# Kernel tuning notes

Measured on AMD Instinct MI355X. Metric: run time of the kernel, lower is better.

The kernel has to match this reference:

```python
import jax, jax.numpy as jnp
import numpy as np

IN_DIM = 256
OUT_DIM = 256


def setup_inputs() -> dict:
    key = jax.random.key(0)
    k1, k2, k3, k4 = jax.random.split(key, 4)
    B, N = 8, 2048
    X = jax.random.normal(k1, (B, N, IN_DIM), dtype=jnp.float32)
    adj = jax.random.uniform(k2, (B, N, N), dtype=jnp.float32)
    # nn.Linear(input_dim, output_dim): W is [out, in], bias [out]
    bound = 1.0 / np.sqrt(IN_DIM)
    W = jax.random.uniform(k3, (OUT_DIM, IN_DIM), minval=-bound, maxval=bound, dtype=jnp.float32)
    b = jax.random.uniform(k4, (OUT_DIM,), minval=-bound, maxval=bound, dtype=jnp.float32)
    return {"X": X, "adj": adj, "W": W, "b": b}


def reference(X, adj, W, b):
    N = adj.shape[-1]
    # adj_hat = adj + I
    adj_hat = adj + jnp.eye(N, dtype=adj.dtype)
    # D^{-1/2} A_hat D^{-1/2}: diag matmuls are just row/col scaling
    d = jnp.sum(adj_hat, axis=-1) ** -0.5  # [B, N]
    adj_norm = d[..., :, None] * adj_hat * d[..., None, :]
    # aggregate then linear + relu
    H = jnp.matmul(adj_norm, X)  # [B, N, F_in]
    out = jnp.einsum('bnf,of->bno', H, W) + b
    return jax.nn.relu(out)
```

## Files before the change

### kernel.cpp

```cpp
#include <hip/hip_runtime.h>
#include <stdint.h>

typedef __attribute__((ext_vector_type(8))) short bf16x8;
typedef __attribute__((ext_vector_type(8))) unsigned short u16x8;
typedef __attribute__((ext_vector_type(4))) float f32x4;
typedef unsigned short u16;

constexpr int NN = 2048, NF = 256;

__device__ inline u16 f2bf(float f) {
  uint32_t u = __builtin_bit_cast(uint32_t, f);
  uint32_t r = (u + 0x7FFFu + ((u >> 16) & 1u)) >> 16;
  return (u16)r;
}
__device__ inline float bf2f(u16 h) {
  uint32_t u = ((uint32_t)h) << 16;
  return __builtin_bit_cast(float, u);
}

__device__ inline void gload_lds16(const void* g, void* l) {
  __builtin_amdgcn_global_load_lds(
      (const __attribute__((address_space(1))) uint32_t*)g,
      (__attribute__((address_space(3))) uint32_t*)l,
      16, 0, 0);
}

__global__ __launch_bounds__(256) void k_rowsum(const float* __restrict__ adj,
                                                float* __restrict__ d,
                                                const float* __restrict__ W,
                                                u16* __restrict__ Wb) {
  if (blockIdx.x >= 16384) {
    int i = (blockIdx.x - 16384) * 256 + threadIdx.x;
    float4 v = ((const float4*)W)[i];
    ushort4 o;
    o.x = f2bf(v.x); o.y = f2bf(v.y); o.z = f2bf(v.z); o.w = f2bf(v.w);
    *(ushort4*)(Wb + (size_t)i * 4) = o;
    return;
  }
  int row = blockIdx.x;
  const float4* p = (const float4*)(adj + (size_t)row * NN);
  float s = 0.f;
#pragma unroll
  for (int c = 0; c < 2; ++c) {
    float4 v = p[threadIdx.x + 256 * c];
    s += v.x + v.y + v.z + v.w;
  }
#pragma unroll
  for (int off = 32; off > 0; off >>= 1) s += __shfl_down(s, off, 64);
  __shared__ float red[4];
  int lane = threadIdx.x & 63, w = threadIdx.x >> 6;
  if (lane == 0) red[w] = s;
  __syncthreads();
  if (threadIdx.x == 0) {
    float t = red[0] + red[1] + red[2] + red[3] + 1.0f;
    d[row] = 1.0f / sqrtf(t);
  }
}

__global__ __launch_bounds__(256) void k_xprep(const float* __restrict__ X,
                                               const float* __restrict__ d,
                                               u16* __restrict__ XpT) {
  int jt = blockIdx.x, ft = blockIdx.y, b = blockIdx.z;
  int j0 = jt * 64, f0 = ft * 64;
  __shared__ u16 T[64][66];
  int t = threadIdx.x;
#pragma unroll
  for (int s = 0; s < 4; ++s) {
    int q = s * 256 + t;
    int r = q >> 4, c4 = q & 15;
    int j = j0 + r;
    float dv = d[b * NN + j];
    float4 v = *(const float4*)(X + ((size_t)(b * NN + j)) * NF + f0 + c4 * 4);
    T[r][c4 * 4 + 0] = f2bf(v.x * dv);
    T[r][c4 * 4 + 1] = f2bf(v.y * dv);
    T[r][c4 * 4 + 2] = f2bf(v.z * dv);
    T[r][c4 * 4 + 3] = f2bf(v.w * dv);
  }
  __syncthreads();
#pragma unroll
  for (int s = 0; s < 4; ++s) {
    int q = s * 256 + t;
    int fr = q >> 4, c4 = q & 15;
    ushort4 o;
    o.x = T[c4 * 4 + 0][fr]; o.y = T[c4 * 4 + 1][fr];
    o.z = T[c4 * 4 + 2][fr]; o.w = T[c4 * 4 + 3][fr];
    *(ushort4*)(XpT + ((size_t)(b * NF + f0 + fr)) * NN + j0 + c4 * 4) = o;
  }
}

#define BBASE 24576

#define MFMA8(AB, BB)                                                          \
  {                                                                            \
    bf16x8 af0 = *(const bf16x8*)((AB) + aoff0);                               \
    bf16x8 af1 = *(const bf16x8*)((AB) + aoff0 + 1024);                        \
    bf16x8 b0 = *(const bf16x8*)((BB) + boff0);                                \
    bf16x8 b1 = *(const bf16x8*)((BB) + boff0 + 1024);                         \
    bf16x8 b2 = *(const bf16x8*)((BB) + boff0 + 2048);                         \
    bf16x8 b3 = *(const bf16x8*)((BB) + boff0 + 3072);                         \
    asm volatile("s_waitcnt lgkmcnt(0)" ::: "memory");                         \
    __builtin_amdgcn_sched_barrier(0);                                         \
    __builtin_amdgcn_s_setprio(1);                                             \
    acc[0][0] = __builtin_amdgcn_mfma_f32_16x16x32_bf16(af0, b0, acc[0][0], 0, 0, 0); \
    acc[0][1] = __builtin_amdgcn_mfma_f32_16x16x32_bf16(af0, b1, acc[0][1], 0, 0, 0); \
    acc[0][2] = __builtin_amdgcn_mfma_f32_16x16x32_bf16(af0, b2, acc[0][2], 0, 0, 0); \
    acc[0][3] = __builtin_amdgcn_mfma_f32_16x16x32_bf16(af0, b3, acc[0][3], 0, 0, 0); \
    acc[1][0] = __builtin_amdgcn_mfma_f32_16x16x32_bf16(af1, b0, acc[1][0], 0, 0, 0); \
    acc[1][1] = __builtin_amdgcn_mfma_f32_16x16x32_bf16(af1, b1, acc[1][1], 0, 0, 0); \
    acc[1][2] = __builtin_amdgcn_mfma_f32_16x16x32_bf16(af1, b2, acc[1][2], 0, 0, 0); \
    acc[1][3] = __builtin_amdgcn_mfma_f32_16x16x32_bf16(af1, b3, acc[1][3], 0, 0, 0); \
    __builtin_amdgcn_s_setprio(0);                                             \
  }

#define PAIR(G, RG, WG, SN, SW, BR0, BR1, BW0, BW1, VMC0, VMC1, IA, WA, IB0, IB1) \
  {                                                                            \
                                                 \
    if (IB0) {                                                                 \
      gload_lds16(b_src0 + (size_t)(2 * (G) + 2) * 32,                         \
                  smem + BBASE + (BW0) * 16384 + bw0);                         \
      gload_lds16(b_src1 + (size_t)(2 * (G) + 2) * 32,                         \
                  smem + BBASE + (BW0) * 16384 + bw1);                         \
    }                                                                          \
    if (IA) {                                                                  \
      aN0[SN] = *(const float4*)(a_gsrc + (size_t)((G) + 4) * 64);             \
      aN1[SN] = *(const float4*)(a_gsrc + (size_t)((G) + 4) * 64 + 4);         \
    }                                                                          \
    __builtin_amdgcn_sched_barrier(0);                                         \
    asm volatile("s_waitcnt vmcnt(" VMC0 ") lgkmcnt(0)" ::: "memory");         \
    __builtin_amdgcn_sched_barrier(0);                                         \
    __builtin_amdgcn_s_barrier();                                              \
    __builtin_amdgcn_sched_barrier(0);                                         \
    MFMA8(smem + (RG) * 8192, smem + BBASE + (BR0) * 16384)                    \
    __builtin_amdgcn_sched_barrier(0);                                         \
    if (WA) {                                                                  \
      float4 c0 = aN0[SW], c1 = aN1[SW];                                       \
      u16x8 pk;                                                                \
      pk[0] = f2bf(c0.x); pk[1] = f2bf(c0.y); pk[2] = f2bf(c0.z);              \
      pk[3] = f2bf(c0.w); pk[4] = f2bf(c1.x); pk[5] = f2bf(c1.y);              \
      pk[6] = f2bf(c1.z); pk[7] = f2bf(c1.w);                                  \
      *(u16x8*)(smem + (WG) * 8192 + a_ldst) = pk;                             \
    }                                                                          \
    __builtin_amdgcn_sched_barrier(0);                                         \
                                                \
    if (IB1) {                                                                 \
      gload_lds16(b_src0 + (size_t)(2 * (G) + 3) * 32,                         \
                  smem + BBASE + (BW1) * 16384 + bw0);                         \
      gload_lds16(b_src1 + (size_t)(2 * (G) + 3) * 32,                         \
                  smem + BBASE + (BW1) * 16384 + bw1);                         \
    }                                                                          \
    __builtin_amdgcn_sched_barrier(0);                                         \
    asm volatile("s_waitcnt vmcnt(" VMC1 ") lgkmcnt(0)" ::: "memory");         \
    __builtin_amdgcn_sched_barrier(0);                                         \
    __builtin_amdgcn_s_barrier();                                              \
    __builtin_amdgcn_sched_barrier(0);                                         \
    MFMA8(smem + (RG) * 8192 + 4096, smem + BBASE + (BR1) * 16384)             \
    __builtin_amdgcn_sched_barrier(0);                                         \
  }

__global__ __launch_bounds__(512, 2) void k_fused(
    const float* __restrict__ adj, const u16* __restrict__ XpT,
    const float* __restrict__ dsc, const u16* __restrict__ Wb,
    const float* __restrict__ bias, float* __restrict__ out) {
  int flat = blockIdx.x;
  int b = flat & 7, mt = flat >> 3;
  int i0 = mt * 64;

  __shared__ __align__(16) char smem[90112];
  u16* Hs = (u16*)smem;

  int t = threadIdx.x;
  int lane = t & 63, w = t >> 6;
  int l15 = lane & 15, l4 = lane >> 4;
  int wr = w >> 2, wc = w & 3;

  const float* adjf = adj + ((size_t)b * NN + i0) * NN;
  const u16* XpTb = XpT + (size_t)b * NF * NN;

  int rA = t >> 3, kc = t & 7;
  const float* a_gsrc = adjf + (size_t)rA * NN + kc * 8;
  int a_ldst = (kc >> 2) * 4096 + rA * 64 + (((kc & 3) ^ ((rA >> 1) & 3)) << 4);

  int n0s = t >> 2, c0s = t & 3;
  const u16* b_src0 = XpTb + (size_t)n0s * NN + ((c0s ^ ((n0s >> 1) & 3)) << 3);
  int s1 = 512 + t;
  int n1s = s1 >> 2, c1s = s1 & 3;
  const u16* b_src1 = XpTb + (size_t)n1s * NN + ((c1s ^ ((n1s >> 1) & 3)) << 3);
  int bw0 = w << 10;
  int bw1 = 8192 + (w << 10);

  int swz = (l4 ^ ((l15 >> 1) & 3)) << 4;
  int aoff0 = wr * 2048 + l15 * 64 + swz;
  int boff0 = (wc * 64 + l15) * 64 + swz;

  f32x4 acc[2][4] = {};
  float4 aN0[3], aN1[3];

  {
    float4 p0a = *(const float4*)(a_gsrc);
    float4 p0b = *(const float4*)(a_gsrc + 4);
    float4 p1a = *(const float4*)(a_gsrc + 64);
    float4 p1b = *(const float4*)(a_gsrc + 68);
    __builtin_amdgcn_sched_barrier(0);
    gload_lds16(b_src0, smem + BBASE + bw0);
    gload_lds16(b_src1, smem + BBASE + bw1);
    gload_lds16(b_src0 + 32, smem + BBASE + 16384 + bw0);
    gload_lds16(b_src1 + 32, smem + BBASE + 16384 + bw1);
    __builtin_amdgcn_sched_barrier(0);
    aN0[1] = *(const float4*)(a_gsrc + 128);
    aN1[1] = *(const float4*)(a_gsrc + 132);
    aN0[2] = *(const float4*)(a_gsrc + 192);
    aN1[2] = *(const float4*)(a_gsrc + 196);
    __builtin_amdgcn_sched_barrier(0);
    u16x8 pk;
    pk[0] = f2bf(p0a.x); pk[1] = f2bf(p0a.y); pk[2] = f2bf(p0a.z);
    pk[3] = f2bf(p0a.w); pk[4] = f2bf(p0b.x); pk[5] = f2bf(p0b.y);
    pk[6] = f2bf(p0b.z); pk[7] = f2bf(p0b.w);
    *(u16x8*)(smem + a_ldst) = pk;
    pk[0] = f2bf(p1a.x); pk[1] = f2bf(p1a.y); pk[2] = f2bf(p1a.z);
    pk[3] = f2bf(p1a.w); pk[4] = f2bf(p1b.x); pk[5] = f2bf(p1b.y);
    pk[6] = f2bf(p1b.z); pk[7] = f2bf(p1b.w);
    *(u16x8*)(smem + 8192 + a_ldst) = pk;
    __builtin_amdgcn_sched_barrier(0);
  }

  for (int gb = 0; gb < 24; gb += 6) {
    PAIR(gb + 0, 0, 2, 0, 1, 0, 1, 2, 3, "8", "6", 1, 1, 1, 1)
    PAIR(gb + 1, 1, 0, 1, 2, 2, 3, 0, 1, "8", "6", 1, 1, 1, 1)
    PAIR(gb + 2, 2, 1, 2, 0, 0, 1, 2, 3, "8", "6", 1, 1, 1, 1)
    PAIR(gb + 3, 0, 2, 0, 1, 2, 3, 0, 1, "8", "6", 1, 1, 1, 1)
    PAIR(gb + 4, 1, 0, 1, 2, 0, 1, 2, 3, "8", "6", 1, 1, 1, 1)
    PAIR(gb + 5, 2, 1, 2, 0, 2, 3, 0, 1, "8", "6", 1, 1, 1, 1)
  }
  PAIR(24, 0, 2, 0, 1, 0, 1, 2, 3, "8", "6", 1, 1, 1, 1)
  PAIR(25, 1, 0, 1, 2, 2, 3, 0, 1, "8", "6", 1, 1, 1, 1)
  PAIR(26, 2, 1, 2, 0, 0, 1, 2, 3, "8", "6", 1, 1, 1, 1)
  PAIR(27, 0, 2, 0, 1, 2, 3, 0, 1, "8", "6", 1, 1, 1, 1)
  PAIR(28, 1, 0, 1, 2, 0, 1, 2, 3, "6", "4", 0, 1, 1, 1)
  PAIR(29, 2, 1, 2, 0, 2, 3, 0, 1, "4", "4", 0, 1, 1, 1)
  PAIR(30, 0, 2, 0, 1, 0, 1, 2, 3, "4", "4", 0, 0, 1, 1)
  PAIR(31, 1, 0, 1, 2, 2, 3, 0, 1, "2", "0", 0, 0, 0, 0)

  __syncthreads();

  const float* db = dsc + b * NN;
#pragma unroll
  for (int mi = 0; mi < 2; ++mi) {
#pragma unroll
    for (int ni = 0; ni < 4; ++ni) {
      int f = wc * 64 + ni * 16 + l15;
      ushort4 xv = *(const ushort4*)(XpTb + (size_t)f * NN + i0 +
                                     wr * 32 + mi * 16 + l4 * 4);
#pragma unroll
      for (int qq = 0; qq < 4; ++qq) {
        int il = wr * 32 + mi * 16 + l4 * 4 + qq;
        float dv = db[i0 + il];
        float xpv = bf2f(((const u16*)&xv)[qq]);
        float hv = dv * (acc[mi][ni][qq] + xpv);
        Hs[il * 264 + f] = f2bf(hv);
      }
    }
  }
  __syncthreads();

  f32x4 acc2[2][4] = {};
#pragma unroll
  for (int kk = 0; kk < 256; kk += 32) {
    bf16x8 a2[2], b2[4];
#pragma unroll
    for (int mi = 0; mi < 2; ++mi) {
      int r = wr * 32 + mi * 16 + l15;
      a2[mi] = *(const bf16x8*)&Hs[r * 264 + kk + l4 * 8];
    }
#pragma unroll
    for (int ni = 0; ni < 4; ++ni) {
      int o = wc * 64 + ni * 16 + l15;
      b2[ni] = *(const bf16x8*)&Wb[(size_t)o * 256 + kk + l4 * 8];
    }
#pragma unroll
    for (int mi = 0; mi < 2; ++mi)
#pragma unroll
      for (int ni = 0; ni < 4; ++ni)
        acc2[mi][ni] = __builtin_amdgcn_mfma_f32_16x16x32_bf16(a2[mi], b2[ni],
                                                               acc2[mi][ni], 0, 0, 0);
  }

  float* outb = out + ((size_t)b * NN + i0) * NF;
#pragma unroll
  for (int mi = 0; mi < 2; ++mi) {
#pragma unroll
    for (int qq = 0; qq < 4; ++qq) {
      int il = wr * 32 + mi * 16 + l4 * 4 + qq;
#pragma unroll
      for (int ni = 0; ni < 4; ++ni) {
        int o = wc * 64 + ni * 16 + l15;
        float v = acc2[mi][ni][qq] + bias[o];
        outb[(size_t)il * NF + o] = fmaxf(v, 0.f);
      }
    }
  }
}

extern "C" void kernel_launch(void* const* d_in, const int* in_sizes, int n_in,
                              void* d_out, int out_size, void* d_ws, size_t ws_size,
                              hipStream_t stream) {
  const float* X    = (const float*)d_in[0];
  const float* adj  = (const float*)d_in[1];
  const float* W    = (const float*)d_in[2];
  const float* bias = (const float*)d_in[3];
  float* out = (float*)d_out;

  char* ws = (char*)d_ws;
  float* dsc = (float*)(ws);
  u16*   Wb  = (u16*)(ws + 65536);
  u16*   XpT = (u16*)(ws + 262144);

  k_rowsum<<<dim3(16448), dim3(256), 0, stream>>>(adj, dsc, W, Wb);
  k_xprep<<<dim3(32, 4, 8), dim3(256), 0, stream>>>(X, dsc, XpT);
  k_fused<<<dim3(256), dim3(512), 0, stream>>>(adj, XpT, dsc, Wb, bias, out);
}
```

Baseline: 73.14 us.

## Deepen B-operand LDS pipeline from four to six stages

Grows the shared-memory ring for the bf16 X tiles from four to six 16KB slots. The prologue now preloads four B sub-tiles, and each PAIR prefetches two sub-tiles further ahead, with the vmcnt waits and the unrolled schedule retuned to match. The aim is to hide more global-load latency behind the MFMA work. The cost is 120KB of LDS per block, which likely no longer allows two 512-thread blocks per CU as the launch bounds request, so occupancy may drop.

New measurement: 74.20 us. Within noise of the previous version (+1.4%).

```diff
diff --git a/kernel.cpp b/kernel.cpp
--- a/kernel.cpp
+++ b/kernel.cpp
@@ -112,18 +112,18 @@
     __builtin_amdgcn_s_setprio(0);                                             \
   }
 
-#define PAIR(G, RG, WG, SN, SW, BR0, BR1, BW0, BW1, VMC0, VMC1, IA, WA, IB0, IB1) \
+#define PAIR(G, RG, WG, SN, SW, BR0, BR1, BW0, BW1, VMC0, VMC1, IA, WA, IB)    \
   {                                                                            \
-                                                 \
-    if (IB0) {                                                                 \
-      gload_lds16(b_src0 + (size_t)(2 * (G) + 2) * 32,                         \
-                  smem + BBASE + (BW0) * 16384 + bw0);                         \
-      gload_lds16(b_src1 + (size_t)(2 * (G) + 2) * 32,                         \
-                  smem + BBASE + (BW0) * 16384 + bw1);                         \
-    }                                                                          \
+                   \
     if (IA) {                                                                  \
       aN0[SN] = *(const float4*)(a_gsrc + (size_t)((G) + 4) * 64);             \
       aN1[SN] = *(const float4*)(a_gsrc + (size_t)((G) + 4) * 64 + 4);         \
+    }                                                                          \
+    if (IB) {                                                                  \
+      gload_lds16(b_src0 + (size_t)(2 * (G) + 4) * 32,                         \
+                  smem + BBASE + (BW0) * 16384 + bw0);                         \
+      gload_lds16(b_src1 + (size_t)(2 * (G) + 4) * 32,                         \
+                  smem + BBASE + (BW0) * 16384 + bw1);                         \
     }                                                                          \
     __builtin_amdgcn_sched_barrier(0);                                         \
     asm volatile("s_waitcnt vmcnt(" VMC0 ") lgkmcnt(0)" ::: "memory");         \
@@ -142,10 +142,10 @@
     }                                                                          \
     __builtin_amdgcn_sched_barrier(0);                                         \
                                                 \
-    if (IB1) {                                                                 \
-      gload_lds16(b_src0 + (size_t)(2 * (G) + 3) * 32,                         \
+    if (IB) {                                                                  \
+      gload_lds16(b_src0 + (size_t)(2 * (G) + 5) * 32,                         \
                   smem + BBASE + (BW1) * 16384 + bw0);                         \
-      gload_lds16(b_src1 + (size_t)(2 * (G) + 3) * 32,                         \
+      gload_lds16(b_src1 + (size_t)(2 * (G) + 5) * 32,                         \
                   smem + BBASE + (BW1) * 16384 + bw1);                         \
     }                                                                          \
     __builtin_amdgcn_sched_barrier(0);                                         \
@@ -165,7 +165,7 @@
   int b = flat & 7, mt = flat >> 3;
   int i0 = mt * 64;
 
-  __shared__ __align__(16) char smem[90112];
+  __shared__ __align__(16) char smem[122880];
   u16* Hs = (u16*)smem;
 
   int t = threadIdx.x;
@@ -205,6 +205,10 @@
     gload_lds16(b_src1, smem + BBASE + bw1);
     gload_lds16(b_src0 + 32, smem + BBASE + 16384 + bw0);
     gload_lds16(b_src1 + 32, smem + BBASE + 16384 + bw1);
+    gload_lds16(b_src0 + 64, smem + BBASE + 32768 + bw0);
+    gload_lds16(b_src1 + 64, smem + BBASE + 32768 + bw1);
+    gload_lds16(b_src0 + 96, smem + BBASE + 49152 + bw0);
+    gload_lds16(b_src1 + 96, smem + BBASE + 49152 + bw1);
     __builtin_amdgcn_sched_barrier(0);
     aN0[1] = *(const float4*)(a_gsrc + 128);
     aN1[1] = *(const float4*)(a_gsrc + 132);
@@ -223,22 +227,16 @@
     __builtin_amdgcn_sched_barrier(0);
   }
 
-  for (int gb = 0; gb < 24; gb += 6) {
-    PAIR(gb + 0, 0, 2, 0, 1, 0, 1, 2, 3, "8", "6", 1, 1, 1, 1)
-    PAIR(gb + 1, 1, 0, 1, 2, 2, 3, 0, 1, "8", "6", 1, 1, 1, 1)
-    PAIR(gb + 2, 2, 1, 2, 0, 0, 1, 2, 3, "8", "6", 1, 1, 1, 1)
-    PAIR(gb + 3, 0, 2, 0, 1, 2, 3, 0, 1, "8", "6", 1, 1, 1, 1)
-    PAIR(gb + 4, 1, 0, 1, 2, 0, 1, 2, 3, "8", "6", 1, 1, 1, 1)
-    PAIR(gb + 5, 2, 1, 2, 0, 2, 3, 0, 1, "8", "6", 1, 1, 1, 1)
-  }
-  PAIR(24, 0, 2, 0, 1, 0, 1, 2, 3, "8", "6", 1, 1, 1, 1)
-  PAIR(25, 1, 0, 1, 2, 2, 3, 0, 1, "8", "6", 1, 1, 1, 1)
-  PAIR(26, 2, 1, 2, 0, 0, 1, 2, 3, "8", "6", 1, 1, 1, 1)
-  PAIR(27, 0, 2, 0, 1, 2, 3, 0, 1, "8", "6", 1, 1, 1, 1)
-  PAIR(28, 1, 0, 1, 2, 0, 1, 2, 3, "6", "4", 0, 1, 1, 1)
-  PAIR(29, 2, 1, 2, 0, 2, 3, 0, 1, "4", "4", 0, 1, 1, 1)
-  PAIR(30, 0, 2, 0, 1, 0, 1, 2, 3, "4", "4", 0, 0, 1, 1)
-  PAIR(31, 1, 0, 1, 2, 2, 3, 0, 1, "2", "0", 0, 0, 0, 0)
+  for (int gb = 0; gb < 27; gb += 3) {
+    PAIR(gb + 0, 0, 2, 0, 1, 0, 1, 4, 5, "12", "12", 1, 1, 1)
+    PAIR(gb + 1, 1, 0, 1, 2, 2, 3, 0, 1, "12", "12", 1, 1, 1)
+    PAIR(gb + 2, 2, 1, 2, 0, 4, 5, 2, 3, "12", "12", 1, 1, 1)
+  }
+  PAIR(27, 0, 2, 0, 1, 0, 1, 4, 5, "12", "12", 1, 1, 1)
+  PAIR(28, 1, 0, 1, 2, 2, 3, 0, 1, "10", "10", 0, 1, 1)
+  PAIR(29, 2, 1, 2, 0, 4, 5, 2, 3, "8", "8", 0, 1, 1)
+  PAIR(30, 0, 2, 0, 1, 0, 1, 4, 5, "6", "4", 0, 0, 0)
+  PAIR(31, 1, 0, 1, 2, 2, 3, 0, 1, "2", "0", 0, 0, 0)
 
   __syncthreads();
 
```

## Merge prep kernels by moving column scaling into fused GEMM A-load

Applied to the files above, without the earlier changes.

The X transpose/convert no longer depends on the degree vector, so it is merged with the rowsum and W conversion into a single pre-kernel, which removes one launch and its serialization. The column scaling d_j is applied instead to adj elements as they are converted to bf16 inside the fused kernel, which adds extra loads of d and multiplies to the main loop. The main loop is restructured to process two B k-slices per step with one barrier instead of two, using a larger B ring and more LDS. The self-loop term is adjusted to dv*dv*x.

Measured after the change: 78.08 us. +6.8%, slower.

```diff
diff --git a/kernel.cpp b/kernel.cpp
--- a/kernel.cpp
+++ b/kernel.cpp
@@ -25,147 +25,154 @@
       16, 0, 0);
 }
 
-__global__ __launch_bounds__(256) void k_rowsum(const float* __restrict__ adj,
-                                                float* __restrict__ d,
-                                                const float* __restrict__ W,
-                                                u16* __restrict__ Wb) {
-  if (blockIdx.x >= 16384) {
-    int i = (blockIdx.x - 16384) * 256 + threadIdx.x;
+__global__ __launch_bounds__(256) void k_pre(const float* __restrict__ adj,
+                                             float* __restrict__ d,
+                                             const float* __restrict__ X,
+                                             u16* __restrict__ YpT,
+                                             const float* __restrict__ W,
+                                             u16* __restrict__ Wb) {
+  __shared__ u16 T[64][66];
+  __shared__ float red[4];
+  int bx = blockIdx.x, t = threadIdx.x;
+
+  if (bx < 1024) {
+    int jt = bx & 31, ft = (bx >> 5) & 3, b = bx >> 7;
+    int j0 = jt * 64, f0 = ft * 64;
+#pragma unroll
+    for (int s = 0; s < 4; ++s) {
+      int q = s * 256 + t;
+      int r = q >> 4, c4 = q & 15;
+      int j = j0 + r;
+      float4 v = *(const float4*)(X + ((size_t)(b * NN + j)) * NF + f0 + c4 * 4);
+      T[r][c4 * 4 + 0] = f2bf(v.x);
+      T[r][c4 * 4 + 1] = f2bf(v.y);
+      T[r][c4 * 4 + 2] = f2bf(v.z);
+      T[r][c4 * 4 + 3] = f2bf(v.w);
+    }
+    __syncthreads();
+#pragma unroll
+    for (int s = 0; s < 4; ++s) {
+      int q = s * 256 + t;
+      int fr = q >> 4, c4 = q & 15;
+      ushort4 o;
+      o.x = T[c4 * 4 + 0][fr]; o.y = T[c4 * 4 + 1][fr];
+      o.z = T[c4 * 4 + 2][fr]; o.w = T[c4 * 4 + 3][fr];
+      *(ushort4*)(YpT + ((size_t)(b * NF + f0 + fr)) * NN + j0 + c4 * 4) = o;
+    }
+    return;
+  }
+  if (bx < 1088) {
+    int i = (bx - 1024) * 256 + t;
     float4 v = ((const float4*)W)[i];
     ushort4 o;
     o.x = f2bf(v.x); o.y = f2bf(v.y); o.z = f2bf(v.z); o.w = f2bf(v.w);
     *(ushort4*)(Wb + (size_t)i * 4) = o;
     return;
   }
-  int row = blockIdx.x;
+  int row = bx - 1088;
   const float4* p = (const float4*)(adj + (size_t)row * NN);
   float s = 0.f;
 #pragma unroll
   for (int c = 0; c < 2; ++c) {
-    float4 v = p[threadIdx.x + 256 * c];
+    float4 v = p[t + 256 * c];
     s += v.x + v.y + v.z + v.w;
   }
 #pragma unroll
   for (int off = 32; off > 0; off >>= 1) s += __shfl_down(s, off, 64);
-  __shared__ float red[4];
-  int lane = threadIdx.x & 63, w = threadIdx.x >> 6;
+  int lane = t & 63, w = t >> 6;
   if (lane == 0) red[w] = s;
   __syncthreads();
-  if (threadIdx.x == 0) {
-    float t = red[0] + red[1] + red[2] + red[3] + 1.0f;
-    d[row] = 1.0f / sqrtf(t);
-  }
-}
-
-__global__ __launch_bounds__(256) void k_xprep(const float* __restrict__ X,
-                                               const float* __restrict__ d,
-                                               u16* __restrict__ XpT) {
-  int jt = blockIdx.x, ft = blockIdx.y, b = blockIdx.z;
-  int j0 = jt * 64, f0 = ft * 64;
-  __shared__ u16 T[64][66];
-  int t = threadIdx.x;
-#pragma unroll
-  for (int s = 0; s < 4; ++s) {
-    int q = s * 256 + t;
-    int r = q >> 4, c4 = q & 15;
-    int j = j0 + r;
-    float dv = d[b * NN + j];
-    float4 v = *(const float4*)(X + ((size_t)(b * NN + j)) * NF + f0 + c4 * 4);
-    T[r][c4 * 4 + 0] = f2bf(v.x * dv);
-    T[r][c4 * 4 + 1] = f2bf(v.y * dv);
-    T[r][c4 * 4 + 2] = f2bf(v.z * dv);
-    T[r][c4 * 4 + 3] = f2bf(v.w * dv);
-  }
-  __syncthreads();
-#pragma unroll
-  for (int s = 0; s < 4; ++s) {
-    int q = s * 256 + t;
-    int fr = q >> 4, c4 = q & 15;
-    ushort4 o;
-    o.x = T[c4 * 4 + 0][fr]; o.y = T[c4 * 4 + 1][fr];
-    o.z = T[c4 * 4 + 2][fr]; o.w = T[c4 * 4 + 3][fr];
-    *(ushort4*)(XpT + ((size_t)(b * NF + f0 + fr)) * NN + j0 + c4 * 4) = o;
+  if (t == 0) {
+    float tt = red[0] + red[1] + red[2] + red[3] + 1.0f;
+    d[row] = 1.0f / sqrtf(tt);
   }
 }
 
 #define BBASE 24576
 
-#define MFMA8(AB, BB)                                                          \
+#define MFMA8X(A0, A1, B0, B1, B2, B3)                                         \
+    __builtin_amdgcn_s_setprio(1);                                             \
+    acc[0][0] = __builtin_amdgcn_mfma_f32_16x16x32_bf16(A0, B0, acc[0][0], 0, 0, 0); \
+    acc[0][1] = __builtin_amdgcn_mfma_f32_16x16x32_bf16(A0, B1, acc[0][1], 0, 0, 0); \
+    acc[0][2] = __builtin_amdgcn_mfma_f32_16x16x32_bf16(A0, B2, acc[0][2], 0, 0, 0); \
+    acc[0][3] = __builtin_amdgcn_mfma_f32_16x16x32_bf16(A0, B3, acc[0][3], 0, 0, 0); \
+    acc[1][0] = __builtin_amdgcn_mfma_f32_16x16x32_bf16(A1, B0, acc[1][0], 0, 0, 0); \
+    acc[1][1] = __builtin_amdgcn_mfma_f32_16x16x32_bf16(A1, B1, acc[1][1], 0, 0, 0); \
+    acc[1][2] = __builtin_amdgcn_mfma_f32_16x16x32_bf16(A1, B2, acc[1][2], 0, 0, 0); \
+    acc[1][3] = __builtin_amdgcn_mfma_f32_16x16x32_bf16(A1, B3, acc[1][3], 0, 0, 0); \
+    __builtin_amdgcn_s_setprio(0);
+
+#define AWRITED(S, G_)                                                         \
+    {                                                                          \
+      float4 c0 = aN0[S], c1 = aN1[S], e0 = dN0[S], e1 = dN1[S];               \
+      u16x8 pk;                                                                \
+      pk[0] = f2bf(c0.x * e0.x); pk[1] = f2bf(c0.y * e0.y);                    \
+      pk[2] = f2bf(c0.z * e0.z); pk[3] = f2bf(c0.w * e0.w);                    \
+      pk[4] = f2bf(c1.x * e1.x); pk[5] = f2bf(c1.y * e1.y);                    \
+      pk[6] = f2bf(c1.z * e1.z); pk[7] = f2bf(c1.w * e1.w);                    \
+      *(u16x8*)(smem + (G_) * 8192 + a_ldst) = pk;                             \
+    }
+
+#define PAIRX(G, RG, GW, SL, BRB, BWB, VMC, IA, WA, IB)                        \
   {                                                                            \
-    bf16x8 af0 = *(const bf16x8*)((AB) + aoff0);                               \
-    bf16x8 af1 = *(const bf16x8*)((AB) + aoff0 + 1024);                        \
-    bf16x8 b0 = *(const bf16x8*)((BB) + boff0);                                \
-    bf16x8 b1 = *(const bf16x8*)((BB) + boff0 + 1024);                         \
-    bf16x8 b2 = *(const bf16x8*)((BB) + boff0 + 2048);                         \
-    bf16x8 b3 = *(const bf16x8*)((BB) + boff0 + 3072);                         \
-    asm volatile("s_waitcnt lgkmcnt(0)" ::: "memory");                         \
-    __builtin_amdgcn_sched_barrier(0);                                         \
-    __builtin_amdgcn_s_setprio(1);                                             \
-    acc[0][0] = __builtin_amdgcn_mfma_f32_16x16x32_bf16(af0, b0, acc[0][0], 0, 0, 0); \
-    acc[0][1] = __builtin_amdgcn_mfma_f32_16x16x32_bf16(af0, b1, acc[0][1], 0, 0, 0); \
-    acc[0][2] = __builtin_amdgcn_mfma_f32_16x16x32_bf16(af0, b2, acc[0][2], 0, 0, 0); \
-    acc[0][3] = __builtin_amdgcn_mfma_f32_16x16x32_bf16(af0, b3, acc[0][3], 0, 0, 0); \
-    acc[1][0] = __builtin_amdgcn_mfma_f32_16x16x32_bf16(af1, b0, acc[1][0], 0, 0, 0); \
-    acc[1][1] = __builtin_amdgcn_mfma_f32_16x16x32_bf16(af1, b1, acc[1][1], 0, 0, 0); \
-    acc[1][2] = __builtin_amdgcn_mfma_f32_16x16x32_bf16(af1, b2, acc[1][2], 0, 0, 0); \
-    acc[1][3] = __builtin_amdgcn_mfma_f32_16x16x32_bf16(af1, b3, acc[1][3], 0, 0, 0); \
-    __builtin_amdgcn_s_setprio(0);                                             \
-  }
-
-#define PAIR(G, RG, WG, SN, SW, BR0, BR1, BW0, BW1, VMC0, VMC1, IA, WA, IB0, IB1) \
-  {                                                                            \
-                                                 \
-    if (IB0) {                                                                 \
+    if (IB) {                                                                  \
       gload_lds16(b_src0 + (size_t)(2 * (G) + 2) * 32,                         \
-                  smem + BBASE + (BW0) * 16384 + bw0);                         \
+                  smem + BBASE + (BWB) * 16384 + bw0);                         \
       gload_lds16(b_src1 + (size_t)(2 * (G) + 2) * 32,                         \
-                  smem + BBASE + (BW0) * 16384 + bw1);                         \
+                  smem + BBASE + (BWB) * 16384 + bw1);                         \
+      gload_lds16(b_src0 + (size_t)(2 * (G) + 3) * 32,                         \
+                  smem + BBASE + ((BWB) + 1) * 16384 + bw0);                   \
+      gload_lds16(b_src1 + (size_t)(2 * (G) + 3) * 32,                         \
+                  smem + BBASE + ((BWB) + 1) * 16384 + bw1);                   \
     }                                                                          \
     if (IA) {                                                                  \
-      aN0[SN] = *(const float4*)(a_gsrc + (size_t)((G) + 4) * 64);             \
-      aN1[SN] = *(const float4*)(a_gsrc + (size_t)((G) + 4) * 64 + 4);         \
+      aN0[SL] = *(const float4*)(a_gsrc + (size_t)((G) + 4) * 64);             \
+      aN1[SL] = *(const float4*)(a_gsrc + (size_t)((G) + 4) * 64 + 4);         \
+      dN0[SL] = *(const float4*)(d_gsrc + (size_t)((G) + 4) * 64);             \
+      dN1[SL] = *(const float4*)(d_gsrc + (size_t)((G) + 4) * 64 + 4);         \
     }                                                                          \
     __builtin_amdgcn_sched_barrier(0);                                         \
-    asm volatile("s_waitcnt vmcnt(" VMC0 ") lgkmcnt(0)" ::: "memory");         \
+    asm volatile("s_waitcnt vmcnt(" VMC ")" ::: "memory");                     \
     __builtin_amdgcn_sched_barrier(0);                                         \
     __builtin_amdgcn_s_barrier();                                              \
     __builtin_amdgcn_sched_barrier(0);                                         \
-    MFMA8(smem + (RG) * 8192, smem + BBASE + (BR0) * 16384)                    \
-    __builtin_amdgcn_sched_barrier(0);                                         \
-    if (WA) {                                                                  \
-      float4 c0 = aN0[SW], c1 = aN1[SW];                                       \
-      u16x8 pk;                                                                \
-      pk[0] = f2bf(c0.x); pk[1] = f2bf(c0.y); pk[2] = f2bf(c0.z);              \
-      pk[3] = f2bf(c0.w); pk[4] = f2bf(c1.x); pk[5] = f2bf(c1.y);              \
-      pk[6] = f2bf(c1.z); pk[7] = f2bf(c1.w);                                  \
-      *(u16x8*)(smem + (WG) * 8192 + a_ldst) = pk;                             \
-    }                                                                          \
-    __builtin_amdgcn_sched_barrier(0);                                         \
-                                                \
-    if (IB1) {                                                                 \
-      gload_lds16(b_src0 + (size_t)(2 * (G) + 3) * 32,                         \
-                  smem + BBASE + (BW1) * 16384 + bw0);                         \
-      gload_lds16(b_src1 + (size_t)(2 * (G) + 3) * 32,                         \
-                  smem + BBASE + (BW1) * 16384 + bw1);                         \
-    }                                                                          \
-    __builtin_amdgcn_sched_barrier(0);                                         \
-    asm volatile("s_waitcnt vmcnt(" VMC1 ") lgkmcnt(0)" ::: "memory");         \
-    __builtin_amdgcn_sched_barrier(0);                                         \
-    __builtin_amdgcn_s_barrier();                                              \
-    __builtin_amdgcn_sched_barrier(0);                                         \
-    MFMA8(smem + (RG) * 8192 + 4096, smem + BBASE + (BR1) * 16384)             \
+    const char* Ab = smem + (RG) * 8192;                                       \
+    const char* Be = smem + BBASE + (BRB) * 16384;                             \
+    const char* Bo = smem + BBASE + ((BRB) + 1) * 16384;                       \
+    bf16x8 a00 = *(const bf16x8*)(Ab + aoff0);                                 \
+    bf16x8 a01 = *(const bf16x8*)(Ab + aoff0 + 1024);                          \
+    bf16x8 be0 = *(const bf16x8*)(Be + boff0);                                 \
+    bf16x8 be1 = *(const bf16x8*)(Be + boff0 + 1024);                          \
+    bf16x8 be2 = *(const bf16x8*)(Be + boff0 + 2048);                          \
+    bf16x8 be3 = *(const bf16x8*)(Be + boff0 + 3072);                          \
+    __builtin_amdgcn_sched_barrier(0);                                         \
+    bf16x8 a10 = *(const bf16x8*)(Ab + 4096 + aoff0);                          \
+    bf16x8 a11 = *(const bf16x8*)(Ab + 4096 + aoff0 + 1024);                   \
+    bf16x8 bo0 = *(const bf16x8*)(Bo + boff0);                                 \
+    bf16x8 bo1 = *(const bf16x8*)(Bo + boff0 + 1024);                          \
+    bf16x8 bo2 = *(const bf16x8*)(Bo + boff0 + 2048);                          \
+    bf16x8 bo3 = *(const bf16x8*)(Bo + boff0 + 3072);                          \
+    asm volatile("s_waitcnt lgkmcnt(6)" ::: "memory");                         \
+    __builtin_amdgcn_sched_barrier(0);                                         \
+    MFMA8X(a00, a01, be0, be1, be2, be3)                                       \
+    __builtin_amdgcn_sched_barrier(0);                                         \
+    asm volatile("s_waitcnt lgkmcnt(0)" ::: "memory");                         \
+    __builtin_amdgcn_sched_barrier(0);                                         \
+    MFMA8X(a10, a11, bo0, bo1, bo2, bo3)                                       \
+    __builtin_amdgcn_sched_barrier(0);                                         \
+    if (WA) { AWRITED(GW, GW) }                                                \
     __builtin_amdgcn_sched_barrier(0);                                         \
   }
 
 __global__ __launch_bounds__(512, 2) void k_fused(
-    const float* __restrict__ adj, const u16* __restrict__ XpT,
+    const float* __restrict__ adj, const u16* __restrict__ YpT,
     const float* __restrict__ dsc, const u16* __restrict__ Wb,
     const float* __restrict__ bias, float* __restrict__ out) {
   int flat = blockIdx.x;
   int b = flat & 7, mt = flat >> 3;
   int i0 = mt * 64;
 
-  __shared__ __align__(16) char smem[90112];
+  __shared__ __align__(16) char smem[122880];
   u16* Hs = (u16*)smem;
 
   int t = threadIdx.x;
@@ -174,17 +181,18 @@
   int wr = w >> 2, wc = w & 3;
 
   const float* adjf = adj + ((size_t)b * NN + i0) * NN;
-  const u16* XpTb = XpT + (size_t)b * NF * NN;
+  const u16* YpTb = YpT + (size_t)b * NF * NN;
 
   int rA = t >> 3, kc = t & 7;
   const float* a_gsrc = adjf + (size_t)rA * NN + kc * 8;
+  const float* d_gsrc = dsc + b * NN + kc * 8;
   int a_ldst = (kc >> 2) * 4096 + rA * 64 + (((kc & 3) ^ ((rA >> 1) & 3)) << 4);
 
   int n0s = t >> 2, c0s = t & 3;
-  const u16* b_src0 = XpTb + (size_t)n0s * NN + ((c0s ^ ((n0s >> 1) & 3)) << 3);
+  const u16* b_src0 = YpTb + (size_t)n0s * NN + ((c0s ^ ((n0s >> 1) & 3)) << 3);
   int s1 = 512 + t;
   int n1s = s1 >> 2, c1s = s1 & 3;
-  const u16* b_src1 = XpTb + (size_t)n1s * NN + ((c1s ^ ((n1s >> 1) & 3)) << 3);
+  const u16* b_src1 = YpTb + (size_t)n1s * NN + ((c1s ^ ((n1s >> 1) & 3)) << 3);
   int bw0 = w << 10;
   int bw1 = 8192 + (w << 10);
 
@@ -193,52 +201,61 @@
   int boff0 = (wc * 64 + l15) * 64 + swz;
 
   f32x4 acc[2][4] = {};
-  float4 aN0[3], aN1[3];
+  float4 aN0[3], aN1[3], dN0[3], dN1[3];
 
   {
     float4 p0a = *(const float4*)(a_gsrc);
     float4 p0b = *(const float4*)(a_gsrc + 4);
     float4 p1a = *(const float4*)(a_gsrc + 64);
     float4 p1b = *(const float4*)(a_gsrc + 68);
+    float4 q0a = *(const float4*)(d_gsrc);
+    float4 q0b = *(const float4*)(d_gsrc + 4);
+    float4 q1a = *(const float4*)(d_gsrc + 64);
+    float4 q1b = *(const float4*)(d_gsrc + 68);
     __builtin_amdgcn_sched_barrier(0);
     gload_lds16(b_src0, smem + BBASE + bw0);
     gload_lds16(b_src1, smem + BBASE + bw1);
     gload_lds16(b_src0 + 32, smem + BBASE + 16384 + bw0);
     gload_lds16(b_src1 + 32, smem + BBASE + 16384 + bw1);
     __builtin_amdgcn_sched_barrier(0);
-    aN0[1] = *(const float4*)(a_gsrc + 128);
-    aN1[1] = *(const float4*)(a_gsrc + 132);
-    aN0[2] = *(const float4*)(a_gsrc + 192);
-    aN1[2] = *(const float4*)(a_gsrc + 196);
+    aN0[2] = *(const float4*)(a_gsrc + 128);
+    aN1[2] = *(const float4*)(a_gsrc + 132);
+    dN0[2] = *(const float4*)(d_gsrc + 128);
+    dN1[2] = *(const float4*)(d_gsrc + 132);
+    aN0[0] = *(const float4*)(a_gsrc + 192);
+    aN1[0] = *(const float4*)(a_gsrc + 196);
+    dN0[0] = *(const float4*)(d_gsrc + 192);
+    dN1[0] = *(const float4*)(d_gsrc + 196);
     __builtin_amdgcn_sched_barrier(0);
     u16x8 pk;
-    pk[0] = f2bf(p0a.x); pk[1] = f2bf(p0a.y); pk[2] = f2bf(p0a.z);
-    pk[3] = f2bf(p0a.w); pk[4] = f2bf(p0b.x); pk[5] = f2bf(p0b.y);
-    pk[6] = f2bf(p0b.z); pk[7] = f2bf(p0b.w);
+    pk[0] = f2bf(p0a.x * q0a.x); pk[1] = f2bf(p0a.y * q0a.y);
+    pk[2] = f2bf(p0a.z * q0a.z); pk[3] = f2bf(p0a.w * q0a.w);
+    pk[4] = f2bf(p0b.x * q0b.x); pk[5] = f2bf(p0b.y * q0b.y);
+    pk[6] = f2bf(p0b.z * q0b.z); pk[7] = f2bf(p0b.w * q0b.w);
     *(u16x8*)(smem + a_ldst) = pk;
-    pk[0] = f2bf(p1a.x); pk[1] = f2bf(p1a.y); pk[2] = f2bf(p1a.z);
-    pk[3] = f2bf(p1a.w); pk[4] = f2bf(p1b.x); pk[5] = f2bf(p1b.y);
-    pk[6] = f2bf(p1b.z); pk[7] = f2bf(p1b.w);
+    pk[0] = f2bf(p1a.x * q1a.x); pk[1] = f2bf(p1a.y * q1a.y);
+    pk[2] = f2bf(p1a.z * q1a.z); pk[3] = f2bf(p1a.w * q1a.w);
+    pk[4] = f2bf(p1b.x * q1b.x); pk[5] = f2bf(p1b.y * q1b.y);
+    pk[6] = f2bf(p1b.z * q1b.z); pk[7] = f2bf(p1b.w * q1b.w);
     *(u16x8*)(smem + 8192 + a_ldst) = pk;
+    asm volatile("s_waitcnt lgkmcnt(0)" ::: "memory");
     __builtin_amdgcn_sched_barrier(0);
   }
 
-  for (int gb = 0; gb < 24; gb += 6) {
-    PAIR(gb + 0, 0, 2, 0, 1, 0, 1, 2, 3, "8", "6", 1, 1, 1, 1)
-    PAIR(gb + 1, 1, 0, 1, 2, 2, 3, 0, 1, "8", "6", 1, 1, 1, 1)
-    PAIR(gb + 2, 2, 1, 2, 0, 0, 1, 2, 3, "8", "6", 1, 1, 1, 1)
-    PAIR(gb + 3, 0, 2, 0, 1, 2, 3, 0, 1, "8", "6", 1, 1, 1, 1)
-    PAIR(gb + 4, 1, 0, 1, 2, 0, 1, 2, 3, "8", "6", 1, 1, 1, 1)
-    PAIR(gb + 5, 2, 1, 2, 0, 2, 3, 0, 1, "8", "6", 1, 1, 1, 1)
-  }
-  PAIR(24, 0, 2, 0, 1, 0, 1, 2, 3, "8", "6", 1, 1, 1, 1)
-  PAIR(25, 1, 0, 1, 2, 2, 3, 0, 1, "8", "6", 1, 1, 1, 1)
-  PAIR(26, 2, 1, 2, 0, 0, 1, 2, 3, "8", "6", 1, 1, 1, 1)
-  PAIR(27, 0, 2, 0, 1, 2, 3, 0, 1, "8", "6", 1, 1, 1, 1)
-  PAIR(28, 1, 0, 1, 2, 0, 1, 2, 3, "6", "4", 0, 1, 1, 1)
-  PAIR(29, 2, 1, 2, 0, 2, 3, 0, 1, "4", "4", 0, 1, 1, 1)
-  PAIR(30, 0, 2, 0, 1, 0, 1, 2, 3, "4", "4", 0, 0, 1, 1)
-  PAIR(31, 1, 0, 1, 2, 2, 3, 0, 1, "2", "0", 0, 0, 0, 0)
+  PAIRX(0, 0, 2, 1, 0, 2, "16", 1, 1, 1)
+  PAIRX(1, 1, 0, 2, 2, 4, "12", 1, 1, 1)
+  PAIRX(2, 2, 1, 0, 4, 0, "12", 1, 1, 1)
+  for (int gb = 1; gb < 9; ++gb) {
+    int g = gb * 3;
+    PAIRX(g + 0, 0, 2, 1, 0, 2, "12", 1, 1, 1)
+    PAIRX(g + 1, 1, 0, 2, 2, 4, "12", 1, 1, 1)
+    PAIRX(g + 2, 2, 1, 0, 4, 0, "12", 1, 1, 1)
+  }
+  PAIRX(27, 0, 2, 1, 0, 2, "12", 1, 1, 1)
+  PAIRX(28, 1, 0, 2, 2, 4, "8", 0, 1, 1)
+  PAIRX(29, 2, 1, 0, 4, 0, "4", 0, 1, 1)
+  PAIRX(30, 0, 2, 1, 0, 2, "4", 0, 0, 1)
+  PAIRX(31, 1, 0, 2, 2, 4, "0", 0, 0, 0)
 
   __syncthreads();
 
@@ -248,14 +265,14 @@
 #pragma unroll
     for (int ni = 0; ni < 4; ++ni) {
       int f = wc * 64 + ni * 16 + l15;
-      ushort4 xv = *(const ushort4*)(XpTb + (size_t)f * NN + i0 +
+      ushort4 xv = *(const ushort4*)(YpTb + (size_t)f * NN + i0 +
                                      wr * 32 + mi * 16 + l4 * 4);
 #pragma unroll
       for (int qq = 0; qq < 4; ++qq) {
         int il = wr * 32 + mi * 16 + l4 * 4 + qq;
         float dv = db[i0 + il];
         float xpv = bf2f(((const u16*)&xv)[qq]);
-        float hv = dv * (acc[mi][ni][qq] + xpv);
+        float hv = dv * (acc[mi][ni][qq] + dv * xpv);
         Hs[il * 264 + f] = f2bf(hv);
       }
     }
@@ -312,9 +329,8 @@
   char* ws = (char*)d_ws;
   float* dsc = (float*)(ws);
   u16*   Wb  = (u16*)(ws + 65536);
-  u16*   XpT = (u16*)(ws + 262144);
-
-  k_rowsum<<<dim3(16448), dim3(256), 0, stream>>>(adj, dsc, W, Wb);
-  k_xprep<<<dim3(32, 4, 8), dim3(256), 0, stream>>>(X, dsc, XpT);
-  k_fused<<<dim3(256), dim3(512), 0, stream>>>(adj, XpT, dsc, Wb, bias, out);
-}
+  u16*   YpT = (u16*)(ws + 262144);
+
+  k_pre<<<dim3(17472), dim3(256), 0, stream>>>(adj, dsc, X, YpT, W, Wb);
+  k_fused<<<dim3(256), dim3(512), 0, stream>>>(adj, YpT, dsc, Wb, bias, out);
+}
```
